# Optimization experiments

Hardware: AMD Instinct MI355X
Metric: run time of the kernel (lower is better)

Reference implementation:

```python
import jax, jax.numpy as jnp
import numpy as np

N_CLASS = 81          # 80 foreground classes + background (class 0)
R = 1000              # test-time RoIs from RPN
IMG_H, IMG_W = 600.0, 800.0   # original_size
SCORE_THRESH = 0.05
NMS_THRESH = 0.5
LOC_STD = jnp.array([0.1, 0.1, 0.2, 0.2], dtype=jnp.float32)
LOC_MEAN = jnp.zeros(4, dtype=jnp.float32)


def setup_inputs() -> dict:
    key = jax.random.key(0)
    k1, k2, k3, k4 = jax.random.split(key, 4)
    # rois in (ymin, xmin, ymax, xmax) within the image
    yx = jax.random.uniform(k1, (R, 2), dtype=jnp.float32) * jnp.array([IMG_H * 0.8, IMG_W * 0.8])
    hw = jax.random.uniform(k2, (R, 2), dtype=jnp.float32) * jnp.array([IMG_H * 0.2, IMG_W * 0.2]) + 1.0
    roi = jnp.concatenate([yx, yx + hw], axis=1)                       # [R, 4]
    roi_loc = jax.random.normal(k3, (R, N_CLASS * 4), dtype=jnp.float32)
    roi_score = jax.random.normal(k4, (R, N_CLASS), dtype=jnp.float32) * 2.0
    return {"roi": roi, "roi_loc": roi_loc, "roi_score": roi_score}


def _loc2bbox(roi, loc):
    # roi [R,4] (ymin,xmin,ymax,xmax); loc [R,C,4] (dy,dx,dh,dw) -> bbox [R,C,4]
    h = roi[:, 2] - roi[:, 0]
    w = roi[:, 3] - roi[:, 1]
    cy = roi[:, 0] + 0.5 * h
    cx = roi[:, 1] + 0.5 * w
    dy, dx, dh, dw = loc[..., 0], loc[..., 1], loc[..., 2], loc[..., 3]
    ctr_y = dy * h[:, None] + cy[:, None]
    ctr_x = dx * w[:, None] + cx[:, None]
    nh = jnp.exp(dh) * h[:, None]
    nw = jnp.exp(dw) * w[:, None]
    return jnp.stack([ctr_y - 0.5 * nh, ctr_x - 0.5 * nw,
                      ctr_y + 0.5 * nh, ctr_x + 0.5 * nw], axis=-1)


def _nms_per_class(boxes, scores):
    # boxes [R,4], scores [R] -> (sorted boxes, sorted scores, keep mask)
    order = jnp.argsort(-scores)
    b = boxes[order]
    s = scores[order]
    valid = s > SCORE_THRESH
    area = (b[:, 2] - b[:, 0]) * (b[:, 3] - b[:, 1])
    tl = jnp.maximum(b[:, None, :2], b[None, :, :2])
    br = jnp.minimum(b[:, None, 2:], b[None, :, 2:])
    wh = jnp.clip(br - tl, 0.0)
    inter = wh[..., 0] * wh[..., 1]
    iou = inter / (area[:, None] + area[None, :] - inter + 1e-9)   # [R,R]
    idx = jnp.arange(R)

    def body(i, keep):
        sup = keep[i] & (iou[i] > NMS_THRESH) & (idx > i)
        return keep & ~sup

    keep = jax.lax.fori_loop(0, R, body, valid)
    return b, s, keep


def reference(roi, roi_loc, roi_score):
    loc = roi_loc.reshape(R, N_CLASS, 4) * LOC_STD + LOC_MEAN
    bbox = _loc2bbox(roi, loc)                                   # [R, C, 4]
    # clamp: even coords (y) to [0, H], odd coords (x) to [0, W]
    hi = jnp.array([IMG_H, IMG_W, IMG_H, IMG_W], dtype=bbox.dtype)
    bbox = jnp.clip(bbox, 0.0, hi)
    prob = jax.nn.softmax(roi_score, axis=1)                     # [R, C]
    # per-class suppression, skipping background class 0
    boxes_c = jnp.swapaxes(bbox, 0, 1)[1:]                       # [C-1, R, 4]
    scores_c = prob.T[1:]                                        # [C-1, R]
    b, s, keep = jax.vmap(_nms_per_class)(boxes_c, scores_c)
    out = jnp.where(keep[..., None],
                    jnp.concatenate([b, s[..., None]], axis=-1), 0.0)  # [C-1, R, 5]
    labels = jnp.broadcast_to(jnp.arange(N_CLASS - 1, dtype=jnp.int32)[:, None], keep.shape)
    labels = jnp.where(keep, labels, -1)
    return out, labels
```

## Files before the change

### kernel.cpp

```cpp
#include <hip/hip_runtime.h>
#include <math.h>

#define R 1000
#define NC 81
#define CAP 1024
#define NT 512
#define SUPMAX 512
#define WMAX 8
#define PT_LD 1024

__global__ __launch_bounds__(256) void softmax_probT_kernel(
    const float* __restrict__ roi_score,
    float* __restrict__ probT)
{
    const int wid  = threadIdx.x >> 6;
    const int lane = threadIdx.x & 63;
    const int r    = blockIdx.x * 4 + wid;
    if (r >= R) return;
    const float* sc = roi_score + r * NC;
    float v0 = sc[lane];
    float v1 = (lane < NC - 64) ? sc[lane + 64] : -INFINITY;
    float m = fmaxf(v0, v1);
    #pragma unroll
    for (int off = 32; off > 0; off >>= 1)
        m = fmaxf(m, __shfl_xor(m, off, 64));
    float e0 = expf(v0 - m);
    float e1 = (lane < NC - 64) ? expf(v1 - m) : 0.0f;
    float e = e0 + e1;
    #pragma unroll
    for (int off = 32; off > 0; off >>= 1)
        e += __shfl_xor(e, off, 64);
    float rcp = 1.0f / e;
    probT[lane * PT_LD + r] = e0 * rcp;
    if (lane < NC - 64)
        probT[(lane + 64) * PT_LD + r] = e1 * rcp;
}

__global__ __launch_bounds__(NT) void frcnn_class_kernel(
    const float* __restrict__ roi,
    const float* __restrict__ roi_loc,
    const float* __restrict__ probT,
    float* __restrict__ out)
{
    const int c   = blockIdx.x + 1;
    const int tid = threadIdx.x;

    __shared__ float s_score[CAP];
    __shared__ int   s_idx[CAP];
    __shared__ float s_ss[CAP];
    __shared__ float s_y0[CAP], s_x0[CAP], s_y1[CAP], s_x1[CAP], s_area[CAP];
    __shared__ int   s_keepi[CAP];
    __shared__ unsigned long long s_sup[SUPMAX * WMAX];
    __shared__ unsigned long long s_kw[WMAX];
    __shared__ int   s_cnt;

    if (tid == 0) s_cnt = 0;
    __syncthreads();

    const float* pc = probT + c * PT_LD;
    for (int r = tid; r < R; r += NT) {
        float p = pc[r];
        if (p > 0.05f) {
            int slot = atomicAdd(&s_cnt, 1);
            s_score[slot] = p;
            s_idx[slot]   = r;
        }
    }
    __syncthreads();
    const int V = s_cnt;

    for (int p = tid; p < V; p += NT) {
        float sp = s_score[p];
        int   ip = s_idx[p];
        int rank = 0;
        for (int q = 0; q < V; ++q) {
            float sq = s_score[q];
            int   iq = s_idx[q];
            rank += (sq > sp) || (sq == sp && iq < ip);
        }
        float ry0 = roi[ip*4+0], rx0 = roi[ip*4+1];
        float ry1 = roi[ip*4+2], rx1 = roi[ip*4+3];
        float h = ry1 - ry0, w = rx1 - rx0;
        float cy = ry0 + 0.5f*h, cx = rx0 + 0.5f*w;
        const float* lp = roi_loc + (size_t)ip*(NC*4) + c*4;
        float dy = lp[0]*0.1f, dx = lp[1]*0.1f;
        float dh = lp[2]*0.2f, dw = lp[3]*0.2f;
        float ny = dy*h + cy, nx = dx*w + cx;
        float nh = expf(dh)*h, nw = expf(dw)*w;
        float y0 = ny - 0.5f*nh, x0 = nx - 0.5f*nw;
        float y1 = ny + 0.5f*nh, x1 = nx + 0.5f*nw;
        y0 = fminf(fmaxf(y0, 0.f), 600.f);
        x0 = fminf(fmaxf(x0, 0.f), 800.f);
        y1 = fminf(fmaxf(y1, 0.f), 600.f);
        x1 = fminf(fmaxf(x1, 0.f), 800.f);
        s_ss[rank] = sp;
        s_y0[rank] = y0; s_x0[rank] = x0; s_y1[rank] = y1; s_x1[rank] = x1;
        s_area[rank] = (y1 - y0) * (x1 - x0);
        s_keepi[rank] = 1;
    }
    __syncthreads();

    if (V > 0 && V <= SUPMAX) {
        const int W = (V + 63) >> 6;
        for (int i = tid; i < V; i += NT) {
            float ay0 = s_y0[i], ax0 = s_x0[i];
            float ay1 = s_y1[i], ax1 = s_x1[i];
            float aa  = s_area[i];
            for (int w = 0; w < W; ++w) {
                int j0 = w * 64;
                int js = (i + 1 > j0) ? i + 1 : j0;
                int je = (j0 + 64 < V) ? j0 + 64 : V;
                unsigned long long bits = 0ull;
                for (int j = js; j < je; ++j) {
                    float ty = fmaxf(ay0, s_y0[j]);
                    float tx = fmaxf(ax0, s_x0[j]);
                    float by = fminf(ay1, s_y1[j]);
                    float bx = fminf(ax1, s_x1[j]);
                    float hh = fmaxf(by - ty, 0.f);
                    float ww = fmaxf(bx - tx, 0.f);
                    float inter = hh * ww;
                    float iou = inter / (aa + s_area[j] - inter + 1e-9f);
                    if (iou > 0.5f) bits |= (1ull << (j - j0));
                }
                s_sup[i * W + w] = bits;
            }
        }
        __syncthreads();
        if (tid == 0) {
            unsigned long long kw[WMAX];
            #pragma unroll
            for (int w = 0; w < WMAX; ++w) {
                int full = V - w * 64;
                kw[w] = (full >= 64) ? ~0ull : (full > 0 ? ((1ull << full) - 1ull) : 0ull);
            }
            #pragma unroll
            for (int w = 0; w < WMAX; ++w) {
                if (w * 64 < V) {
                    unsigned long long cur = kw[w];
                    int lim = V - w * 64; if (lim > 64) lim = 64;
                    for (int b = 0; b < lim; ++b) {
                        if ((cur >> b) & 1ull) {
                            const unsigned long long* row = &s_sup[(w * 64 + b) * W];
                            cur &= ~row[w];
                            #pragma unroll
                            for (int w2 = 0; w2 < WMAX; ++w2) {
                                if (w2 > w) { if (w2 < W) kw[w2] &= ~row[w2]; }
                            }
                        }
                    }
                    kw[w] = cur;
                }
            }
            #pragma unroll
            for (int w = 0; w < WMAX; ++w) s_kw[w] = kw[w];
        }
        __syncthreads();
    } else if (V > SUPMAX) {
        for (int i = 0; i < V; ++i) {
            if (s_keepi[i]) {
                float ay0 = s_y0[i], ax0 = s_x0[i];
                float ay1 = s_y1[i], ax1 = s_x1[i];
                float aa  = s_area[i];
                for (int jj = i + 1 + tid; jj < V; jj += NT) {
                    float ty = fmaxf(ay0, s_y0[jj]);
                    float tx = fmaxf(ax0, s_x0[jj]);
                    float by = fminf(ay1, s_y1[jj]);
                    float bx = fminf(ax1, s_x1[jj]);
                    float hh = fmaxf(by - ty, 0.f);
                    float ww = fmaxf(bx - tx, 0.f);
                    float inter = hh * ww;
                    float iou = inter / (aa + s_area[jj] - inter + 1e-9f);
                    if (iou > 0.5f) s_keepi[jj] = 0;
                }
            }
            __syncthreads();
        }
    }

    const bool matrix_path = (V <= SUPMAX);
    float* out0 = out + (size_t)(c - 1) * R * 5;
    float* out1 = out + (size_t)80 * R * 5 + (size_t)(c - 1) * R;
    for (int p = tid; p < R; p += NT) {
        bool kept = false;
        if (p < V)
            kept = matrix_path ? (((s_kw[p >> 6] >> (p & 63)) & 1ull) != 0ull)
                               : (s_keepi[p] != 0);
        float y0 = 0.f, x0 = 0.f, y1 = 0.f, x1 = 0.f, s = 0.f, lab = -1.0f;
        if (kept) {
            y0 = s_y0[p]; x0 = s_x0[p]; y1 = s_y1[p]; x1 = s_x1[p];
            s  = s_ss[p];
            lab = (float)(c - 1);
        }
        out0[p*5+0] = y0; out0[p*5+1] = x0; out0[p*5+2] = y1;
        out0[p*5+3] = x1; out0[p*5+4] = s;
        out1[p] = lab;
    }
}

extern "C" void kernel_launch(void* const* d_in, const int* in_sizes, int n_in,
                              void* d_out, int out_size, void* d_ws, size_t ws_size,
                              hipStream_t stream) {
    const float* roi       = (const float*)d_in[0];
    const float* roi_loc   = (const float*)d_in[1];
    const float* roi_score = (const float*)d_in[2];
    float* out   = (float*)d_out;
    float* probT = (float*)d_ws;

    hipLaunchKernelGGL(softmax_probT_kernel, dim3((R + 3) / 4), dim3(256), 0, stream,
                       roi_score, probT);
    hipLaunchKernelGGL(frcnn_class_kernel, dim3(NC - 1), dim3(NT), 0, stream,
                       roi, roi_loc, probT, out);
}
```

Measured before the change: 86.74 us.

## Fuse softmax into NMS kernel via cooperative grid sync; prefetch suppression rows

The separate softmax kernel is merged into the per-class NMS kernel. It runs as a cooperative launch of 80 blocks that first compute the transposed probabilities, then meet at a grid-wide sync before the per-class work. This removes one kernel launch and the gap between the two kernels, at the cost of a grid barrier and a less parallel softmax phase. The serial greedy suppression loop also prefetches the next suppression-mask row into registers, so shared-memory latency overlaps with the current iteration.

Result: slower. 127.7 us (+47.2%).

```diff
diff --git a/kernel.cpp b/kernel.cpp
--- a/kernel.cpp
+++ b/kernel.cpp
@@ -1,49 +1,29 @@
 #include <hip/hip_runtime.h>
+#include <hip/hip_cooperative_groups.h>
 #include <math.h>
+
+namespace cg = cooperative_groups;
 
 #define R 1000
 #define NC 81
 #define CAP 1024
 #define NT 512
+#define NWAVE (NT / 64)
+#define NBLK 80
 #define SUPMAX 512
 #define WMAX 8
 #define PT_LD 1024
 
-__global__ __launch_bounds__(256) void softmax_probT_kernel(
-    const float* __restrict__ roi_score,
-    float* __restrict__ probT)
-{
-    const int wid  = threadIdx.x >> 6;
-    const int lane = threadIdx.x & 63;
-    const int r    = blockIdx.x * 4 + wid;
-    if (r >= R) return;
-    const float* sc = roi_score + r * NC;
-    float v0 = sc[lane];
-    float v1 = (lane < NC - 64) ? sc[lane + 64] : -INFINITY;
-    float m = fmaxf(v0, v1);
-    #pragma unroll
-    for (int off = 32; off > 0; off >>= 1)
-        m = fmaxf(m, __shfl_xor(m, off, 64));
-    float e0 = expf(v0 - m);
-    float e1 = (lane < NC - 64) ? expf(v1 - m) : 0.0f;
-    float e = e0 + e1;
-    #pragma unroll
-    for (int off = 32; off > 0; off >>= 1)
-        e += __shfl_xor(e, off, 64);
-    float rcp = 1.0f / e;
-    probT[lane * PT_LD + r] = e0 * rcp;
-    if (lane < NC - 64)
-        probT[(lane + 64) * PT_LD + r] = e1 * rcp;
-}
-
-__global__ __launch_bounds__(NT) void frcnn_class_kernel(
+__global__ __launch_bounds__(NT) void frcnn_coop_kernel(
     const float* __restrict__ roi,
     const float* __restrict__ roi_loc,
-    const float* __restrict__ probT,
+    const float* __restrict__ roi_score,
+    float* __restrict__ probT,
     float* __restrict__ out)
 {
-    const int c   = blockIdx.x + 1;
-    const int tid = threadIdx.x;
+    const int tid  = threadIdx.x;
+    const int wid  = tid >> 6;
+    const int lane = tid & 63;
 
     __shared__ float s_score[CAP];
     __shared__ int   s_idx[CAP];
@@ -55,7 +35,30 @@
     __shared__ int   s_cnt;
 
     if (tid == 0) s_cnt = 0;
-    __syncthreads();
+
+    for (int r = blockIdx.x * NWAVE + wid; r < R; r += NBLK * NWAVE) {
+        const float* sc = roi_score + r * NC;
+        float v0 = sc[lane];
+        float v1 = (lane < NC - 64) ? sc[lane + 64] : -INFINITY;
+        float m = fmaxf(v0, v1);
+        #pragma unroll
+        for (int off = 32; off > 0; off >>= 1)
+            m = fmaxf(m, __shfl_xor(m, off, 64));
+        float e0 = expf(v0 - m);
+        float e1 = (lane < NC - 64) ? expf(v1 - m) : 0.0f;
+        float e = e0 + e1;
+        #pragma unroll
+        for (int off = 32; off > 0; off >>= 1)
+            e += __shfl_xor(e, off, 64);
+        float rcp = 1.0f / e;
+        probT[lane * PT_LD + r] = e0 * rcp;
+        if (lane < NC - 64)
+            probT[(lane + 64) * PT_LD + r] = e1 * rcp;
+    }
+
+    cg::this_grid().sync();
+
+    const int c = blockIdx.x + 1;
 
     const float* pc = probT + c * PT_LD;
     for (int r = tid; r < R; r += NT) {
@@ -133,20 +136,29 @@
                 int full = V - w * 64;
                 kw[w] = (full >= 64) ? ~0ull : (full > 0 ? ((1ull << full) - 1ull) : 0ull);
             }
+            unsigned long long rowb[WMAX], nxtb[WMAX];
+            #pragma unroll
+            for (int w = 0; w < WMAX; ++w) rowb[w] = (w < W) ? s_sup[w] : 0ull;
             #pragma unroll
             for (int w = 0; w < WMAX; ++w) {
                 if (w * 64 < V) {
                     unsigned long long cur = kw[w];
                     int lim = V - w * 64; if (lim > 64) lim = 64;
                     for (int b = 0; b < lim; ++b) {
+                        int nxt = w * 64 + b + 1;
+                        if (nxt < V) {
+                            #pragma unroll
+                            for (int w2 = 0; w2 < WMAX; ++w2)
+                                if (w2 < W) nxtb[w2] = s_sup[nxt * W + w2];
+                        }
                         if ((cur >> b) & 1ull) {
-                            const unsigned long long* row = &s_sup[(w * 64 + b) * W];
-                            cur &= ~row[w];
+                            cur &= ~rowb[w];
                             #pragma unroll
-                            for (int w2 = 0; w2 < WMAX; ++w2) {
-                                if (w2 > w) { if (w2 < W) kw[w2] &= ~row[w2]; }
-                            }
+                            for (int w2 = 0; w2 < WMAX; ++w2)
+                                if (w2 > w && w2 < W) kw[w2] &= ~rowb[w2];
                         }
+                        #pragma unroll
+                        for (int w2 = 0; w2 < WMAX; ++w2) rowb[w2] = nxtb[w2];
                     }
                     kw[w] = cur;
                 }
@@ -206,8 +218,8 @@
     float* out   = (float*)d_out;
     float* probT = (float*)d_ws;
 
-    hipLaunchKernelGGL(softmax_probT_kernel, dim3((R + 3) / 4), dim3(256), 0, stream,
-                       roi_score, probT);
-    hipLaunchKernelGGL(frcnn_class_kernel, dim3(NC - 1), dim3(NT), 0, stream,
-                       roi, roi_loc, probT, out);
+    void* args[] = { (void*)&roi, (void*)&roi_loc, (void*)&roi_score,
+                     (void*)&probT, (void*)&out };
+    hipLaunchCooperativeKernel((const void*)frcnn_coop_kernel,
+                               dim3(NBLK), dim3(NT), args, 0, stream);
 }
```

## Decode boxes during compaction, prefetch suppression rows, shrink class block size

Applied to the files above, without the earlier changes.

Box decoding moves out of the post-rank phase and into the initial threshold/compaction pass, held in registers and scattered to sorted slots once ranks are known. This overlaps the global roi/roi_loc loads with the filtering step rather than running them after the rank loop. The serial greedy NMS scan now prefetches the next suppression row into registers, taking shared-memory latency off the dependent chain. The per-class block size also drops from 512 to 256 threads, which halves parallelism in the O(V^2) rank and IoU loops.

Result: slower. 96.03 us (+10.7%).

```diff
diff --git a/kernel.cpp b/kernel.cpp
--- a/kernel.cpp
+++ b/kernel.cpp
@@ -4,12 +4,14 @@
 #define R 1000
 #define NC 81
 #define CAP 1024
-#define NT 512
+#define NTA 256
+#define NTB 256
+#define NPASS ((R + NTB - 1) / NTB)
 #define SUPMAX 512
 #define WMAX 8
 #define PT_LD 1024
 
-__global__ __launch_bounds__(256) void softmax_probT_kernel(
+__global__ __launch_bounds__(NTA) void softmax_probT_kernel(
     const float* __restrict__ roi_score,
     float* __restrict__ probT)
 {
@@ -36,7 +38,7 @@
         probT[(lane + 64) * PT_LD + r] = e1 * rcp;
 }
 
-__global__ __launch_bounds__(NT) void frcnn_class_kernel(
+__global__ __launch_bounds__(NTB) void frcnn_classB_kernel(
     const float* __restrict__ roi,
     const float* __restrict__ roi_loc,
     const float* __restrict__ probT,
@@ -45,11 +47,11 @@
     const int c   = blockIdx.x + 1;
     const int tid = threadIdx.x;
 
-    __shared__ float s_score[CAP];
-    __shared__ int   s_idx[CAP];
+    __shared__ float s_sc[CAP];
+    __shared__ int   s_id[CAP];
+    __shared__ int   s_rank[CAP];
     __shared__ float s_ss[CAP];
     __shared__ float s_y0[CAP], s_x0[CAP], s_y1[CAP], s_x1[CAP], s_area[CAP];
-    __shared__ int   s_keepi[CAP];
     __shared__ unsigned long long s_sup[SUPMAX * WMAX];
     __shared__ unsigned long long s_kw[WMAX];
     __shared__ int   s_cnt;
@@ -57,52 +59,73 @@
     if (tid == 0) s_cnt = 0;
     __syncthreads();
 
+    bool  fnd[NPASS];
+    int   slt[NPASS];
+    float qy0[NPASS], qx0[NPASS], qy1[NPASS], qx1[NPASS], qar[NPASS], qsc[NPASS];
     const float* pc = probT + c * PT_LD;
-    for (int r = tid; r < R; r += NT) {
-        float p = pc[r];
-        if (p > 0.05f) {
-            int slot = atomicAdd(&s_cnt, 1);
-            s_score[slot] = p;
-            s_idx[slot]   = r;
+    #pragma unroll
+    for (int ps = 0; ps < NPASS; ++ps) {
+        fnd[ps] = false;
+        int r = tid + ps * NTB;
+        if (r < R) {
+            float p = pc[r];
+            if (p > 0.05f) {
+                int slot = atomicAdd(&s_cnt, 1);
+                s_sc[slot] = p;
+                s_id[slot] = r;
+                float ry0 = roi[r*4+0], rx0 = roi[r*4+1];
+                float ry1 = roi[r*4+2], rx1 = roi[r*4+3];
+                float h = ry1 - ry0, w = rx1 - rx0;
+                float cy = ry0 + 0.5f*h, cx = rx0 + 0.5f*w;
+                const float* lp = roi_loc + (size_t)r*(NC*4) + c*4;
+                float dy = lp[0]*0.1f, dx = lp[1]*0.1f;
+                float dh = lp[2]*0.2f, dw = lp[3]*0.2f;
+                float ny = dy*h + cy, nx = dx*w + cx;
+                float nh = expf(dh)*h, nw = expf(dw)*w;
+                float y0 = ny - 0.5f*nh, x0 = nx - 0.5f*nw;
+                float y1 = ny + 0.5f*nh, x1 = nx + 0.5f*nw;
+                y0 = fminf(fmaxf(y0, 0.f), 600.f);
+                x0 = fminf(fmaxf(x0, 0.f), 800.f);
+                y1 = fminf(fmaxf(y1, 0.f), 600.f);
+                x1 = fminf(fmaxf(x1, 0.f), 800.f);
+                fnd[ps] = true; slt[ps] = slot; qsc[ps] = p;
+                qy0[ps] = y0; qx0[ps] = x0; qy1[ps] = y1; qx1[ps] = x1;
+                qar[ps] = (y1 - y0) * (x1 - x0);
+            }
         }
     }
     __syncthreads();
     const int V = s_cnt;
 
-    for (int p = tid; p < V; p += NT) {
-        float sp = s_score[p];
-        int   ip = s_idx[p];
+    for (int p = tid; p < V; p += NTB) {
+        float sp = s_sc[p];
+        int   ip = s_id[p];
         int rank = 0;
         for (int q = 0; q < V; ++q) {
-            float sq = s_score[q];
-            int   iq = s_idx[q];
+            float sq = s_sc[q];
+            int   iq = s_id[q];
             rank += (sq > sp) || (sq == sp && iq < ip);
         }
-        float ry0 = roi[ip*4+0], rx0 = roi[ip*4+1];
-        float ry1 = roi[ip*4+2], rx1 = roi[ip*4+3];
-        float h = ry1 - ry0, w = rx1 - rx0;
-        float cy = ry0 + 0.5f*h, cx = rx0 + 0.5f*w;
-        const float* lp = roi_loc + (size_t)ip*(NC*4) + c*4;
-        float dy = lp[0]*0.1f, dx = lp[1]*0.1f;
-        float dh = lp[2]*0.2f, dw = lp[3]*0.2f;
-        float ny = dy*h + cy, nx = dx*w + cx;
-        float nh = expf(dh)*h, nw = expf(dw)*w;
-        float y0 = ny - 0.5f*nh, x0 = nx - 0.5f*nw;
-        float y1 = ny + 0.5f*nh, x1 = nx + 0.5f*nw;
-        y0 = fminf(fmaxf(y0, 0.f), 600.f);
-        x0 = fminf(fmaxf(x0, 0.f), 800.f);
-        y1 = fminf(fmaxf(y1, 0.f), 600.f);
-        x1 = fminf(fmaxf(x1, 0.f), 800.f);
-        s_ss[rank] = sp;
-        s_y0[rank] = y0; s_x0[rank] = x0; s_y1[rank] = y1; s_x1[rank] = x1;
-        s_area[rank] = (y1 - y0) * (x1 - x0);
-        s_keepi[rank] = 1;
-    }
-    __syncthreads();
-
+        s_rank[p] = rank;
+    }
+    __syncthreads();
+
+    #pragma unroll
+    for (int ps = 0; ps < NPASS; ++ps) {
+        if (fnd[ps]) {
+            int rk = s_rank[slt[ps]];
+            s_ss[rk]   = qsc[ps];
+            s_y0[rk]   = qy0[ps]; s_x0[rk] = qx0[ps];
+            s_y1[rk]   = qy1[ps]; s_x1[rk] = qx1[ps];
+            s_area[rk] = qar[ps];
+        }
+    }
+    __syncthreads();
+
+    int* s_keepi = s_rank;
     if (V > 0 && V <= SUPMAX) {
         const int W = (V + 63) >> 6;
-        for (int i = tid; i < V; i += NT) {
+        for (int i = tid; i < V; i += NTB) {
             float ay0 = s_y0[i], ax0 = s_x0[i];
             float ay1 = s_y1[i], ax1 = s_x1[i];
             float aa  = s_area[i];
@@ -133,20 +156,29 @@
                 int full = V - w * 64;
                 kw[w] = (full >= 64) ? ~0ull : (full > 0 ? ((1ull << full) - 1ull) : 0ull);
             }
+            unsigned long long rowb[WMAX], nxtb[WMAX];
+            #pragma unroll
+            for (int w = 0; w < WMAX; ++w) rowb[w] = (w < W) ? s_sup[w] : 0ull;
             #pragma unroll
             for (int w = 0; w < WMAX; ++w) {
                 if (w * 64 < V) {
                     unsigned long long cur = kw[w];
                     int lim = V - w * 64; if (lim > 64) lim = 64;
                     for (int b = 0; b < lim; ++b) {
+                        int nxt = w * 64 + b + 1;
+                        if (nxt < V) {
+                            #pragma unroll
+                            for (int w2 = 0; w2 < WMAX; ++w2)
+                                if (w2 < W) nxtb[w2] = s_sup[nxt * W + w2];
+                        }
                         if ((cur >> b) & 1ull) {
-                            const unsigned long long* row = &s_sup[(w * 64 + b) * W];
-                            cur &= ~row[w];
+                            cur &= ~rowb[w];
                             #pragma unroll
-                            for (int w2 = 0; w2 < WMAX; ++w2) {
-                                if (w2 > w) { if (w2 < W) kw[w2] &= ~row[w2]; }
-                            }
+                            for (int w2 = 0; w2 < WMAX; ++w2)
+                                if (w2 > w && w2 < W) kw[w2] &= ~rowb[w2];
                         }
+                        #pragma unroll
+                        for (int w2 = 0; w2 < WMAX; ++w2) rowb[w2] = nxtb[w2];
                     }
                     kw[w] = cur;
                 }
@@ -156,12 +188,14 @@
         }
         __syncthreads();
     } else if (V > SUPMAX) {
+        for (int p = tid; p < V; p += NTB) s_keepi[p] = 1;
+        __syncthreads();
         for (int i = 0; i < V; ++i) {
             if (s_keepi[i]) {
                 float ay0 = s_y0[i], ax0 = s_x0[i];
                 float ay1 = s_y1[i], ax1 = s_x1[i];
                 float aa  = s_area[i];
-                for (int jj = i + 1 + tid; jj < V; jj += NT) {
+                for (int jj = i + 1 + tid; jj < V; jj += NTB) {
                     float ty = fmaxf(ay0, s_y0[jj]);
                     float tx = fmaxf(ax0, s_x0[jj]);
                     float by = fminf(ay1, s_y1[jj]);
@@ -180,7 +214,7 @@
     const bool matrix_path = (V <= SUPMAX);
     float* out0 = out + (size_t)(c - 1) * R * 5;
     float* out1 = out + (size_t)80 * R * 5 + (size_t)(c - 1) * R;
-    for (int p = tid; p < R; p += NT) {
+    for (int p = tid; p < R; p += NTB) {
         bool kept = false;
         if (p < V)
             kept = matrix_path ? (((s_kw[p >> 6] >> (p & 63)) & 1ull) != 0ull)
@@ -206,8 +240,8 @@
     float* out   = (float*)d_out;
     float* probT = (float*)d_ws;
 
-    hipLaunchKernelGGL(softmax_probT_kernel, dim3((R + 3) / 4), dim3(256), 0, stream,
+    hipLaunchKernelGGL(softmax_probT_kernel, dim3((R + 3) / 4), dim3(NTA), 0, stream,
                        roi_score, probT);
-    hipLaunchKernelGGL(frcnn_class_kernel, dim3(NC - 1), dim3(NT), 0, stream,
+    hipLaunchKernelGGL(frcnn_classB_kernel, dim3(NC - 1), dim3(NTB), 0, stream,
                        roi, roi_loc, probT, out);
 }
```
